# Performance work log

Hardware: AMD Instinct MI355X
Metric: run time of the kernel (lower is better)

## Reference

```python
import jax, jax.numpy as jnp
import numpy as np

H = 512  # hidden_size == input_size
L = 2    # num_layers
B = 64   # batch
T = 256  # seq_len


def setup_inputs() -> dict:
    key = jax.random.key(0)
    ks = jax.random.split(key, 16)
    def n(k, shape, mean=0.0, std=1.0):
        return mean + std * jax.random.normal(k, shape, dtype=jnp.float32)
    inp = {
        'seq_len': T,
        'init_h': n(ks[0], (L, B, H)),
        'init_c': n(ks[1], (L, B, H)),
        'eps_w': n(ks[2], (T, H, H)),
        'eps_b': n(ks[3], (T, H)),
        # stacked LSTM cell params (PyTorch LSTMCell layout: [4H, in])
        'W_ih0': n(ks[4], (4 * H, H), std=1.0 / np.sqrt(H)),
        'W_hh0': n(ks[5], (4 * H, H), std=1.0 / np.sqrt(H)),
        'b_ih0': n(ks[6], (4 * H,), std=1.0 / np.sqrt(H)),
        'b_hh0': n(ks[7], (4 * H,), std=1.0 / np.sqrt(H)),
        'W_ih1': n(ks[8], (4 * H, H), std=1.0 / np.sqrt(H)),
        'W_hh1': n(ks[9], (4 * H, H), std=1.0 / np.sqrt(H)),
        'b_ih1': n(ks[10], (4 * H,), std=1.0 / np.sqrt(H)),
        'b_hh1': n(ks[11], (4 * H,), std=1.0 / np.sqrt(H)),
        # BayesianLinear params
        'w_mu': n(ks[12], (H, H), std=0.1),
        'w_log_var': n(ks[13], (H, H), mean=-3.0, std=0.1),
        'b_mu': n(ks[14], (H,), std=0.1),
        'b_log_var': n(ks[15], (H,), mean=-3.0, std=0.1),
    }
    return inp


def _lstm_cell(x, h, c, W_ih, W_hh, b_ih, b_hh):
    gates = x @ W_ih.T + b_ih + h @ W_hh.T + b_hh  # [B, 4H]
    i, f, g, o = jnp.split(gates, 4, axis=-1)
    i = jax.nn.sigmoid(i)
    f = jax.nn.sigmoid(f)
    g = jnp.tanh(g)
    o = jax.nn.sigmoid(o)
    c_new = f * c + i * g
    h_new = o * jnp.tanh(c_new)
    return h_new, c_new


def reference(init_h, init_c, eps_w, eps_b,
              W_ih0, W_hh0, b_ih0, b_hh0,
              W_ih1, W_hh1, b_ih1, b_hh1,
              w_mu, w_log_var, b_mu, b_log_var,
              seq_len):
    batch = init_h.shape[1]
    hidden = init_h.shape[2]
    x0 = jnp.zeros((batch, hidden), dtype=init_h.dtype)
    w_sigma = jnp.exp(0.5 * w_log_var)
    b_sigma = jnp.exp(0.5 * b_log_var)

    def step(carry, eps):
        x, h, c = carry  # h,c: [L, B, H]
        ew, eb = eps
        h0, c0 = _lstm_cell(x, h[0], c[0], W_ih0, W_hh0, b_ih0, b_hh0)
        h1, c1 = _lstm_cell(h0, h[1], c[1], W_ih1, W_hh1, b_ih1, b_hh1)
        # BayesianLinear reparameterized sample per step
        w = w_mu + w_sigma * ew
        b = b_mu + b_sigma * eb
        x_next = h1 @ w.T + b
        h_new = jnp.stack([h0, h1])
        c_new = jnp.stack([c0, c1])
        return (x_next, h_new, c_new), h1

    _, out_features = jax.lax.scan(step, (x0, init_h, init_c), (eps_w, eps_b), length=seq_len)
    return out_features  # [seq_len, B, H] (== stacked list of h_last)
```

## Files before the change

### kernel.cpp

```cpp
#include <hip/hip_runtime.h>
#include <hip/hip_bf16.h>

#define T_STEPS 256
#define BATCH   64
#define HID     512
#define NWG     256
#define NTHR    256

typedef float f32x4 __attribute__((ext_vector_type(4)));
typedef short bf16x8 __attribute__((ext_vector_type(8)));
typedef unsigned long long u64;

#define W0OFF   0u
#define W1OFF   65536u
#define WSTOFF  131072u
#define T1OFF   147456u
#define BNCOFF  148480u
#define EBOFF   148992u
#define SMEM_BYTES 149024

__device__ __forceinline__ short f2b(float f) {
  __hip_bfloat16 h = __float2bfloat16(f);
  return *reinterpret_cast<short*>(&h);
}
__device__ __forceinline__ float b2f(short s) {
  __hip_bfloat16 h;
  *reinterpret_cast<short*>(&h) = s;
  return __bfloat162float(h);
}
__device__ __forceinline__ float sigf(float x) { return 1.0f / (1.0f + __expf(-x)); }
__device__ __forceinline__ float tanh_f(float x) { return 2.0f / (1.0f + __expf(-2.0f * x)) - 1.0f; }

__device__ __forceinline__ bf16x8 pack8(float4 a, float4 b) {
  bf16x8 r;
  r[0] = f2b(a.x); r[1] = f2b(a.y); r[2] = f2b(a.z); r[3] = f2b(a.w);
  r[4] = f2b(b.x); r[5] = f2b(b.y); r[6] = f2b(b.z); r[7] = f2b(b.w);
  return r;
}

__device__ __forceinline__ void g_store16(void* p, bf16x8 v) {
  const u64* s = reinterpret_cast<const u64*>(&v);
  u64* d = reinterpret_cast<u64*>(p);
  __hip_atomic_store(d + 0, s[0], __ATOMIC_RELAXED, __HIP_MEMORY_SCOPE_AGENT);
  __hip_atomic_store(d + 1, s[1], __ATOMIC_RELAXED, __HIP_MEMORY_SCOPE_AGENT);
}
__device__ __forceinline__ bf16x8 g_load16(const void* p) {
  const u64* s = reinterpret_cast<const u64*>(p);
  union { u64 q[2]; bf16x8 v; } u;
  u.q[0] = __hip_atomic_load(s + 0, __ATOMIC_RELAXED, __HIP_MEMORY_SCOPE_AGENT);
  u.q[1] = __hip_atomic_load(s + 1, __ATOMIC_RELAXED, __HIP_MEMORY_SCOPE_AGENT);
  return u.v;
}
__device__ __forceinline__ void g_load_frag(bf16x8* dst, const unsigned short* p) {
#pragma unroll
  for (int i = 0; i < 16; ++i) dst[i] = g_load16(p + (size_t)i * 32);
}

__device__ __forceinline__ void post_flag(unsigned int* p, unsigned int val) {
  asm volatile("s_waitcnt vmcnt(0)" ::: "memory");
  __hip_atomic_store(p, val, __ATOMIC_RELAXED, __HIP_MEMORY_SCOPE_AGENT);
}
__device__ __forceinline__ void poll_flags(const unsigned int* cohort, unsigned int target) {
  const unsigned int* p = cohort + (threadIdx.x & 63);
  for (;;) {
    unsigned int v = __hip_atomic_load(p, __ATOMIC_RELAXED, __HIP_MEMORY_SCOPE_AGENT);
    if (__all((int)(v >= target))) break;
    __builtin_amdgcn_s_sleep(1);
  }
  __builtin_amdgcn_sched_barrier(0);
}

__device__ __forceinline__ void stage_weights(char* smem, unsigned int base,
                                              const float* Wih, const float* Whh,
                                              int u0, int tid) {
  for (int p = tid; p < 4096; p += NTHR) {
    const int row = p >> 7;
    const int col = (p & 127) * 8;
    const int gate = row >> 3;
    const int grow = gate * 512 + u0 + (row & 7);
    const float* src = (col < 512) ? (Wih + (size_t)grow * HID + col)
                                   : (Whh + (size_t)grow * HID + (col - 512));
    float4 v0 = *(const float4*)src;
    float4 v1 = *(const float4*)(src + 4);
    unsigned int byte = base + (unsigned int)row * 2048u + (unsigned int)col * 2u;
    byte ^= (unsigned int)(row & 7) << 4;
    *(bf16x8*)(smem + byte) = pack8(v0, v1);
  }
}

__device__ __forceinline__ void mm_half(const char* smem, const bf16x8* a, unsigned int wOff,
                                        int brow, int colHalf, int koff, f32x4& A0, f32x4& A1) {
  const unsigned int bb = wOff + (unsigned int)brow * 2048u + (unsigned int)colHalf * 2u;
  const unsigned int sw = (unsigned int)(brow & 7) << 4;
#pragma unroll
  for (int ks = 0; ks < 16; ++ks) {
    bf16x8 b = *(const bf16x8*)(smem + ((bb + (unsigned int)((ks * 32 + koff) * 2)) ^ sw));
    if (ks & 1)
      A1 = __builtin_amdgcn_mfma_f32_16x16x32_bf16(a[ks], b, A1, 0, 0, 0);
    else
      A0 = __builtin_amdgcn_mfma_f32_16x16x32_bf16(a[ks], b, A0, 0, 0, 0);
  }
}

__device__ __forceinline__ void cell_update(char* smem, f32x4 acc, float bt0, float bgb,
                                            float bob, float* cst, float* hv, int lane) {
#pragma unroll
  for (int j = 0; j < 4; ++j) acc[j] += bt0;
  float part[4];
#pragma unroll
  for (int j = 0; j < 4; ++j) part[j] = __shfl_xor(acc[j], 8);
  const float* T1 = (const float*)(smem + T1OFF);
  const int cs = lane & 7;
  const int rb = (lane >> 4) * 4;
#pragma unroll
  for (int j = 0; j < 4; ++j) {
    const float iv = acc[j];
    const float fv = part[j];
    const float gv = T1[(rb + j) * 16 + cs] + bgb;
    const float ov = T1[(rb + j) * 16 + cs + 8] + bob;
    const float cn = sigf(fv) * cst[j] + sigf(iv) * tanh_f(gv);
    cst[j] = cn;
    hv[j] = sigf(ov) * tanh_f(cn);
  }
}

extern "C" __global__ void __launch_bounds__(NTHR, 1)
dlstm_kernel(const float* __restrict__ init_h, const float* __restrict__ init_c,
             const float* __restrict__ eps_w, const float* __restrict__ eps_b,
             const float* __restrict__ W_ih0, const float* __restrict__ W_hh0,
             const float* __restrict__ b_ih0, const float* __restrict__ b_hh0,
             const float* __restrict__ W_ih1, const float* __restrict__ W_hh1,
             const float* __restrict__ b_ih1, const float* __restrict__ b_hh1,
             const float* __restrict__ w_mu, const float* __restrict__ w_log_var,
             const float* __restrict__ b_mu, const float* __restrict__ b_log_var,
             float* __restrict__ out, unsigned int* __restrict__ flags,
             unsigned short* __restrict__ xbuf, unsigned short* __restrict__ h0buf,
             unsigned short* __restrict__ h1buf) {
  extern __shared__ char smem[];
  const int tid = threadIdx.x;
  const int bid = blockIdx.x;
  const int bg = bid & 3;
  const int u  = bid >> 2;
  const int u0 = u * 8;
  const int wave = tid >> 6;
  const int lane = tid & 63;
  const int col = lane & 15;
  const int cs = lane & 7;
  const int rb = (lane >> 4) * 4;
  const int koff = (lane >> 4) * 8;
  const bool is_act = col < 8;
  const size_t BH = (size_t)BATCH * HID;
  unsigned int* cohort = flags + bg * 256;
  unsigned int* myflag = cohort + u;
  const int arow = bg * 16 + col;
  const int brow = wave * 16 + col;

  stage_weights(smem, W0OFF, W_ih0, W_hh0, u0, tid);
  stage_weights(smem, W1OFF, W_ih1, W_hh1, u0, tid);
  {
    bf16x8 z = {0, 0, 0, 0, 0, 0, 0, 0};
    for (int p = tid; p < 512; p += NTHR) {
      const int row = 8 + (p >> 6);
      const int c8 = (p & 63) * 8;
      unsigned int byte = WSTOFF + (unsigned int)row * 1024u + (unsigned int)c8 * 2u;
      byte ^= (unsigned int)(row & 7) << 4;
      *(bf16x8*)(smem + byte) = z;
    }
  }
  float bt0_l0 = 0, bt0_l1 = 0, bgb0 = 0, bob0 = 0, bgb1 = 0, bob1 = 0, bmu_l = 0, bsg_l = 0;
  float c0r[4] = {0, 0, 0, 0}, c1r[4] = {0, 0, 0, 0};
  if (wave == 0) {
    const int ofs = (col < 8) ? 0 : 512;
    const int un = u0 + cs;
    bt0_l0 = b_ih0[ofs + un] + b_hh0[ofs + un];
    bt0_l1 = b_ih1[ofs + un] + b_hh1[ofs + un];
    bgb0 = b_ih0[1024 + un] + b_hh0[1024 + un];
    bob0 = b_ih0[1536 + un] + b_hh0[1536 + un];
    bgb1 = b_ih1[1024 + un] + b_hh1[1024 + un];
    bob1 = b_ih1[1536 + un] + b_hh1[1536 + un];
    bmu_l = b_mu[un];
    bsg_l = __expf(0.5f * b_log_var[un]);
    if (is_act) {
#pragma unroll
      for (int j = 0; j < 4; ++j) {
        c0r[j] = init_c[(size_t)(0 * BATCH + bg * 16 + rb + j) * HID + un];
        c1r[j] = init_c[(size_t)(1 * BATCH + bg * 16 + rb + j) * HID + un];
      }
    }
    if (lane < 16) {
      const int row = bg * 16 + lane;
      const float* s0 = init_h + (size_t)row * HID + u0;
      const float* s1 = init_h + (size_t)(BATCH + row) * HID + u0;
      g_store16(h0buf + (size_t)row * HID + u0,
                pack8(*(const float4*)s0, *(const float4*)(s0 + 4)));
      g_store16(h1buf + (size_t)row * HID + u0,
                pack8(*(const float4*)s1, *(const float4*)(s1 + 4)));
      bf16x8 z = {0, 0, 0, 0, 0, 0, 0, 0};
      g_store16(xbuf + (size_t)row * HID + u0, z);
    }
    if (lane == 0) post_flag(myflag, 1u);
  }
  __syncthreads();

#pragma unroll 1
  for (int t = 0; t < T_STEPS; ++t) {
    const int pp = t & 1;
    const unsigned int tb = 3u * (unsigned int)t;

    if (wave >= 2) {
      const int q = tid - 128;
      const int erow = q >> 4;
      const int ecb = (q & 15) * 32;
      const float* pm = w_mu + (size_t)(u0 + erow) * HID + ecb;
      const float* pv = w_log_var + (size_t)(u0 + erow) * HID + ecb;
      const float* pe = eps_w + (size_t)t * HID * HID + (size_t)(u0 + erow) * HID + ecb;
      const unsigned int sw = (unsigned int)erow << 4;
      const unsigned int b0 = WSTOFF + (unsigned int)erow * 1024u + (unsigned int)ecb * 2u;
#pragma unroll
      for (int c = 0; c < 4; ++c) {
        bf16x8 v;
#pragma unroll
        for (int qq = 0; qq < 8; ++qq) {
          const int idx = c * 8 + qq;
          v[qq] = f2b(fmaf(__expf(0.5f * pv[idx]), pe[idx], pm[idx]));
        }
        *(bf16x8*)(smem + ((b0 + (unsigned int)c * 16u) ^ sw)) = v;
      }
      if (wave == 3 && lane < 8)
        ((float*)(smem + EBOFF))[lane] = eps_b[(size_t)t * HID + u0 + lane];
    }

    f32x4 g0 = {0.f, 0.f, 0.f, 0.f};
    if (wave < 2) {
      poll_flags(cohort, tb + 1u);
      bf16x8 sa[16], fa[16];
      g_load_frag(sa, h0buf + (size_t)pp * BH + (size_t)arow * HID + koff);
      g_load_frag(fa, xbuf + (size_t)pp * BH + (size_t)arow * HID + koff);
      f32x4 A0 = {0, 0, 0, 0}, A1 = {0, 0, 0, 0};
      mm_half(smem, sa, W0OFF, brow, 512, koff, A0, A1);
      mm_half(smem, fa, W0OFF, brow, 0, koff, A0, A1);
      g0 = A0 + A1;
      if (wave == 1) {
        float* T1 = (float*)(smem + T1OFF);
#pragma unroll
        for (int j = 0; j < 4; ++j) T1[(rb + j) * 16 + col] = g0[j];
      }
    }
    __syncthreads();
    if (wave == 0) {
      float hv[4];
      cell_update(smem, g0, bt0_l0, bgb0, bob0, c0r, hv, lane);
      float* BNC = (float*)(smem + BNCOFF);
      if (is_act) {
#pragma unroll
        for (int j = 0; j < 4; ++j) BNC[(rb + j) * 8 + cs] = hv[j];
      }
      asm volatile("s_waitcnt lgkmcnt(0)" ::: "memory");
      if (lane < 16) {
        const int row = bg * 16 + lane;
        float4 v0 = *(float4*)(BNC + lane * 8);
        float4 v1 = *(float4*)(BNC + lane * 8 + 4);
        g_store16(h0buf + (size_t)(pp ^ 1) * BH + (size_t)row * HID + u0, pack8(v0, v1));
      }
      if (lane == 0) post_flag(myflag, tb + 2u);
    }

    f32x4 g1 = {0.f, 0.f, 0.f, 0.f};
    if (wave < 2) {
      poll_flags(cohort, tb + 2u);
      bf16x8 sa[16], fa[16];
      g_load_frag(sa, h1buf + (size_t)pp * 2 * BH + (size_t)arow * HID + koff);
      g_load_frag(fa, h0buf + (size_t)(pp ^ 1) * BH + (size_t)arow * HID + koff);
      f32x4 A0 = {0, 0, 0, 0}, A1 = {0, 0, 0, 0};
      mm_half(smem, sa, W1OFF, brow, 512, koff, A0, A1);
      mm_half(smem, fa, W1OFF, brow, 0, koff, A0, A1);
      g1 = A0 + A1;
      if (wave == 1) {
        float* T1 = (float*)(smem + T1OFF);
#pragma unroll
        for (int j = 0; j < 4; ++j) T1[(rb + j) * 16 + col] = g1[j];
      }
    }
    __syncthreads();
    if (wave == 0) {
      float hv[4];
      cell_update(smem, g1, bt0_l1, bgb1, bob1, c1r, hv, lane);
      float* BNC = (float*)(smem + BNCOFF);
      if (is_act) {
#pragma unroll
        for (int j = 0; j < 4; ++j) BNC[(rb + j) * 8 + cs] = hv[j];
      }
      asm volatile("s_waitcnt lgkmcnt(0)" ::: "memory");
      float4 v0 = {0, 0, 0, 0}, v1 = {0, 0, 0, 0};
      if (lane < 16) {
        const int row = bg * 16 + lane;
        v0 = *(float4*)(BNC + lane * 8);
        v1 = *(float4*)(BNC + lane * 8 + 4);
        bf16x8 hi = pack8(v0, v1);
        unsigned short* base = h1buf + (size_t)(pp ^ 1) * 2 * BH;
        g_store16(base + (size_t)row * HID + u0, hi);
        bf16x8 lo;
        const float* va = (const float*)&v0;
        const float* vb = (const float*)&v1;
#pragma unroll
        for (int q = 0; q < 8; ++q) {
          const float f = (q < 4) ? va[q] : vb[q - 4];
          lo[q] = f2b(f - b2f(hi[q]));
        }
        g_store16(base + BH + (size_t)row * HID + u0, lo);
      }
      if (lane == 0) post_flag(myflag, tb + 3u);
      if (lane < 16) {
        const int row = bg * 16 + lane;
        float* od = out + ((size_t)t * BATCH + row) * HID + u0;
        *(float4*)od = v0;
        *(float4*)(od + 4) = v1;
      }
    }

    if (t + 1 < T_STEPS) {
      if (wave == 0) {
        poll_flags(cohort, tb + 3u);
        bf16x8 ahi[16], alo[16];
        const unsigned short* hb =
            h1buf + (size_t)(pp ^ 1) * 2 * BH + (size_t)arow * HID + koff;
        g_load_frag(ahi, hb);
        g_load_frag(alo, hb + BH);
        f32x4 A0 = {0, 0, 0, 0}, A1 = {0, 0, 0, 0};
        const unsigned int bb = WSTOFF + (unsigned int)col * 1024u;
        const unsigned int sw = (unsigned int)(col & 7) << 4;
#pragma unroll
        for (int ks = 0; ks < 16; ++ks) {
          bf16x8 b =
              *(const bf16x8*)(smem + ((bb + (unsigned int)((ks * 32 + koff) * 2)) ^ sw));
          A0 = __builtin_amdgcn_mfma_f32_16x16x32_bf16(ahi[ks], b, A0, 0, 0, 0);
          A1 = __builtin_amdgcn_mfma_f32_16x16x32_bf16(alo[ks], b, A1, 0, 0, 0);
        }
        const float ebv = is_act ? ((const float*)(smem + EBOFF))[cs] : 0.f;
        const float xb = bmu_l + bsg_l * ebv;
        f32x4 a2 = A0 + A1;
        float* BNC = (float*)(smem + BNCOFF);
        if (is_act) {
#pragma unroll
          for (int j = 0; j < 4; ++j) BNC[(rb + j) * 8 + cs] = a2[j] + xb;
        }
        asm volatile("s_waitcnt lgkmcnt(0)" ::: "memory");
        if (lane < 16) {
          const int row = bg * 16 + lane;
          float4 v0 = *(float4*)(BNC + lane * 8);
          float4 v1 = *(float4*)(BNC + lane * 8 + 4);
          g_store16(xbuf + (size_t)(pp ^ 1) * BH + (size_t)row * HID + u0, pack8(v0, v1));
        }
        if (lane == 0) post_flag(myflag, tb + 4u);
      }
      __syncthreads();
    }
  }
}

extern "C" void kernel_launch(void* const* d_in, const int* in_sizes, int n_in, void* d_out,
                              int out_size, void* d_ws, size_t ws_size, hipStream_t stream) {
  const float* init_h = (const float*)d_in[1];
  const float* init_c = (const float*)d_in[2];
  const float* eps_w = (const float*)d_in[3];
  const float* eps_b = (const float*)d_in[4];
  const float* W_ih0 = (const float*)d_in[5];
  const float* W_hh0 = (const float*)d_in[6];
  const float* b_ih0 = (const float*)d_in[7];
  const float* b_hh0 = (const float*)d_in[8];
  const float* W_ih1 = (const float*)d_in[9];
  const float* W_hh1 = (const float*)d_in[10];
  const float* b_ih1 = (const float*)d_in[11];
  const float* b_hh1 = (const float*)d_in[12];
  const float* w_mu = (const float*)d_in[13];
  const float* w_log_var = (const float*)d_in[14];
  const float* b_mu = (const float*)d_in[15];
  const float* b_log_var = (const float*)d_in[16];
  float* out = (float*)d_out;

  unsigned char* ws = (unsigned char*)d_ws;
  unsigned int* flags = (unsigned int*)ws;
  unsigned short* xbuf = (unsigned short*)(ws + 131072);
  unsigned short* h0buf = (unsigned short*)(ws + 262144);
  unsigned short* h1buf = (unsigned short*)(ws + 393216);

  hipMemsetAsync(flags, 0, 4 * 256 * sizeof(unsigned int), stream);
  hipFuncSetAttribute((const void*)dlstm_kernel, hipFuncAttributeMaxDynamicSharedMemorySize,
                      SMEM_BYTES);

  void* args[] = {(void*)&init_h, (void*)&init_c, (void*)&eps_w,  (void*)&eps_b,
                  (void*)&W_ih0,  (void*)&W_hh0,  (void*)&b_ih0,  (void*)&b_hh0,
                  (void*)&W_ih1,  (void*)&W_hh1,  (void*)&b_ih1,  (void*)&b_hh1,
                  (void*)&w_mu,   (void*)&w_log_var, (void*)&b_mu, (void*)&b_log_var,
                  (void*)&out,    (void*)&flags,     (void*)&xbuf, (void*)&h0buf,
                  (void*)&h1buf};
  hipError_t err = hipLaunchCooperativeKernel((void*)dlstm_kernel, dim3(NWG), dim3(NTHR), args,
                                              SMEM_BYTES, stream);
  if (err != hipSuccess) {
    hipLaunchKernelGGL(dlstm_kernel, dim3(NWG), dim3(NTHR), SMEM_BYTES, stream, init_h, init_c,
                       eps_w, eps_b, W_ih0, W_hh0, b_ih0, b_hh0, W_ih1, W_hh1, b_ih1, b_hh1,
                       w_mu, w_log_var, b_mu, b_log_var, out, flags, xbuf, h0buf, h1buf);
  }
}
```

Before: 5.635 ms.

## Prefetch recurrent state fragments early and use cache-bypassing wide loads

Loads of the layer-0 recurrent h fragment are issued at the top of each step, before the eps weight sampling and the flag wait, because that data was written in an earlier phase. The layer-1 recurrent fragment is also loaded during the layer-0 phase. Freshly produced cross-workgroup data is now read with inline-asm global_load_dwordx4 using sc0 sc1 instead of pairs of 64-bit atomic loads. The sleep in the flag spin loop is removed to cut wake-up latency. The costs are more register pressure from the fragment arrays that stay live, busier polling traffic, and a visibility argument for the early loads that depends on the flag protocol ordering.

New measurement: 5.185 ms. 8.0% less time.

```diff
diff --git a/kernel.cpp b/kernel.cpp
--- a/kernel.cpp
+++ b/kernel.cpp
@@ -44,6 +44,32 @@
   __hip_atomic_store(d + 0, s[0], __ATOMIC_RELAXED, __HIP_MEMORY_SCOPE_AGENT);
   __hip_atomic_store(d + 1, s[1], __ATOMIC_RELAXED, __HIP_MEMORY_SCOPE_AGENT);
 }
+__device__ __forceinline__ void llc_load_frag_sync(bf16x8* dst, const unsigned short* p) {
+  asm volatile(
+      "global_load_dwordx4 %0, %16, off sc0 sc1\n\t"
+      "global_load_dwordx4 %1, %16, off offset:64 sc0 sc1\n\t"
+      "global_load_dwordx4 %2, %16, off offset:128 sc0 sc1\n\t"
+      "global_load_dwordx4 %3, %16, off offset:192 sc0 sc1\n\t"
+      "global_load_dwordx4 %4, %16, off offset:256 sc0 sc1\n\t"
+      "global_load_dwordx4 %5, %16, off offset:320 sc0 sc1\n\t"
+      "global_load_dwordx4 %6, %16, off offset:384 sc0 sc1\n\t"
+      "global_load_dwordx4 %7, %16, off offset:448 sc0 sc1\n\t"
+      "global_load_dwordx4 %8, %16, off offset:512 sc0 sc1\n\t"
+      "global_load_dwordx4 %9, %16, off offset:576 sc0 sc1\n\t"
+      "global_load_dwordx4 %10, %16, off offset:640 sc0 sc1\n\t"
+      "global_load_dwordx4 %11, %16, off offset:704 sc0 sc1\n\t"
+      "global_load_dwordx4 %12, %16, off offset:768 sc0 sc1\n\t"
+      "global_load_dwordx4 %13, %16, off offset:832 sc0 sc1\n\t"
+      "global_load_dwordx4 %14, %16, off offset:896 sc0 sc1\n\t"
+      "global_load_dwordx4 %15, %16, off offset:960 sc0 sc1\n\t"
+      "s_waitcnt vmcnt(0)"
+      : "=&v"(dst[0]), "=&v"(dst[1]), "=&v"(dst[2]), "=&v"(dst[3]),
+        "=&v"(dst[4]), "=&v"(dst[5]), "=&v"(dst[6]), "=&v"(dst[7]),
+        "=&v"(dst[8]), "=&v"(dst[9]), "=&v"(dst[10]), "=&v"(dst[11]),
+        "=&v"(dst[12]), "=&v"(dst[13]), "=&v"(dst[14]), "=&v"(dst[15])
+      : "v"(p)
+      : "memory");
+}
 __device__ __forceinline__ bf16x8 g_load16(const void* p) {
   const u64* s = reinterpret_cast<const u64*>(p);
   union { u64 q[2]; bf16x8 v; } u;
@@ -65,7 +91,6 @@
   for (;;) {
     unsigned int v = __hip_atomic_load(p, __ATOMIC_RELAXED, __HIP_MEMORY_SCOPE_AGENT);
     if (__all((int)(v >= target))) break;
-    __builtin_amdgcn_s_sleep(1);
   }
   __builtin_amdgcn_sched_barrier(0);
 }
@@ -207,6 +232,12 @@
     const int pp = t & 1;
     const unsigned int tb = 3u * (unsigned int)t;
 
+    bf16x8 sa[16];
+    if (wave < 2 && t > 0) {
+      g_load_frag(sa, h0buf + (size_t)pp * BH + (size_t)arow * HID + koff);
+      __builtin_amdgcn_sched_barrier(0);
+    }
+
     if (wave >= 2) {
       const int q = tid - 128;
       const int erow = q >> 4;
@@ -231,11 +262,16 @@
     }
 
     f32x4 g0 = {0.f, 0.f, 0.f, 0.f};
+    bf16x8 sth1[16];
     if (wave < 2) {
       poll_flags(cohort, tb + 1u);
-      bf16x8 sa[16], fa[16];
-      g_load_frag(sa, h0buf + (size_t)pp * BH + (size_t)arow * HID + koff);
-      g_load_frag(fa, xbuf + (size_t)pp * BH + (size_t)arow * HID + koff);
+      if (t == 0) {
+        g_load_frag(sa, h0buf + (size_t)pp * BH + (size_t)arow * HID + koff);
+      }
+      bf16x8 fa[16];
+      llc_load_frag_sync(fa, xbuf + (size_t)pp * BH + (size_t)arow * HID + koff);
+      g_load_frag(sth1, h1buf + (size_t)pp * 2 * BH + (size_t)arow * HID + koff);
+      __builtin_amdgcn_sched_barrier(0);
       f32x4 A0 = {0, 0, 0, 0}, A1 = {0, 0, 0, 0};
       mm_half(smem, sa, W0OFF, brow, 512, koff, A0, A1);
       mm_half(smem, fa, W0OFF, brow, 0, koff, A0, A1);
@@ -268,11 +304,10 @@
     f32x4 g1 = {0.f, 0.f, 0.f, 0.f};
     if (wave < 2) {
       poll_flags(cohort, tb + 2u);
-      bf16x8 sa[16], fa[16];
-      g_load_frag(sa, h1buf + (size_t)pp * 2 * BH + (size_t)arow * HID + koff);
-      g_load_frag(fa, h0buf + (size_t)(pp ^ 1) * BH + (size_t)arow * HID + koff);
+      bf16x8 fa[16];
+      llc_load_frag_sync(fa, h0buf + (size_t)(pp ^ 1) * BH + (size_t)arow * HID + koff);
       f32x4 A0 = {0, 0, 0, 0}, A1 = {0, 0, 0, 0};
-      mm_half(smem, sa, W1OFF, brow, 512, koff, A0, A1);
+      mm_half(smem, sth1, W1OFF, brow, 512, koff, A0, A1);
       mm_half(smem, fa, W1OFF, brow, 0, koff, A0, A1);
       g1 = A0 + A1;
       if (wave == 1) {
@@ -324,8 +359,8 @@
         bf16x8 ahi[16], alo[16];
         const unsigned short* hb =
             h1buf + (size_t)(pp ^ 1) * 2 * BH + (size_t)arow * HID + koff;
-        g_load_frag(ahi, hb);
-        g_load_frag(alo, hb + BH);
+        llc_load_frag_sync(ahi, hb);
+        llc_load_frag_sync(alo, hb + BH);
         f32x4 A0 = {0, 0, 0, 0}, A1 = {0, 0, 0, 0};
         const unsigned int bb = WSTOFF + (unsigned int)col * 1024u;
         const unsigned int sw = (unsigned int)(col & 7) << 4;
```
